# Kernel tuning notes

Hardware: AMD Instinct MI355X
Metric: run time of the kernel (lower is better)

Reference implementation:

```python
import jax, jax.numpy as jnp
import numpy as np

N = 50000   # nodes
E = 640000  # edges
D = 128     # feature dim (din == dmid, required since edge_attr is reused every layer)
L = 5       # GINEConv layers
BN_EPS = 1e-5


def setup_inputs() -> dict:
    key = jax.random.key(0)
    ks = jax.random.split(key, 8)
    x = jax.random.normal(ks[0], (N, D), dtype=jnp.float32)
    edge_index = jax.random.randint(ks[1], (2, E), 0, N, dtype=jnp.int64)
    edge_attr = jax.random.normal(ks[2], (E, D), dtype=jnp.float32)
    W1 = jax.random.normal(ks[3], (L, D, D), dtype=jnp.float32) * 0.05
    b1 = jnp.zeros((L, D), dtype=jnp.float32)
    gamma = jnp.ones((L, D), dtype=jnp.float32)
    beta = jnp.zeros((L, D), dtype=jnp.float32)
    W2 = jax.random.normal(ks[4], (L, D, D), dtype=jnp.float32) * 0.05
    b2 = jnp.zeros((L, D), dtype=jnp.float32)
    return {"x": x, "edge_index": edge_index, "edge_attr": edge_attr,
            "W1": W1, "b1": b1, "gamma": gamma, "beta": beta, "W2": W2, "b2": b2}


def reference(x, edge_index, edge_attr, W1, b1, gamma, beta, W2, b2):
    src, dst = edge_index[0], edge_index[1]  # PyG: messages flow src(j) -> dst(i)
    h = x
    for l in range(L):
        # GINEConv message + aggregate: sum_j ReLU(x_j + e_ij)
        m = jax.nn.relu(h[src] + edge_attr)               # [E, D] gather + add
        agg = jax.ops.segment_sum(m, dst, num_segments=N)  # [N, D] scatter-sum
        h = agg + h  # (1 + eps) * x_i with eps = 0
        # MLP: Linear -> BatchNorm1d (batch stats) -> ReLU -> Linear
        h = h @ W1[l] + b1[l]
        mu = jnp.mean(h, axis=0)
        var = jnp.var(h, axis=0)  # biased var, as torch BN uses for normalization
        h = gamma[l] * (h - mu) * jax.lax.rsqrt(var + BN_EPS) + beta[l]
        h = jax.nn.relu(h)
        h = h @ W2[l] + b2[l]
    return h
```

## Files before the change

kernel.cpp:

```cpp
#include <hip/hip_runtime.h>
#include <hip/hip_bf16.h>
#include <stdint.h>

#define D 128
#define LAYERS 5
#define BN_EPS 1e-5f

typedef unsigned int uint32;
typedef __bf16 bf16x8 __attribute__((ext_vector_type(8)));
typedef float f32x4 __attribute__((ext_vector_type(4)));
typedef float f32x2 __attribute__((ext_vector_type(2)));

__device__ inline unsigned short f2bf(float f) {
    uint32 u = __float_as_uint(f);
    return (unsigned short)((u + 0x7fffu + ((u >> 16) & 1u)) >> 16);
}
__device__ inline float bflo(uint32 p) { return __uint_as_float(p << 16); }
__device__ inline float bfhi(uint32 p) { return __uint_as_float(p & 0xffff0000u); }
__device__ inline uint32 pack2(float a, float b) {
    return (uint32)f2bf(a) | ((uint32)f2bf(b) << 16);
}


__global__ void detect_kernel(const int* __restrict__ ei, int* __restrict__ flag) {
    if (threadIdx.x == 0 && blockIdx.x == 0) {
        int allz = 1;
#pragma unroll
        for (int i = 0; i < 16; ++i) allz &= (ei[2 * i + 1] == 0);
        *flag = allz;
    }
}


__global__ __launch_bounds__(256) void hist_kernel(const int* __restrict__ ei,
                                                   const int* __restrict__ flag,
                                                   int* __restrict__ deg, int E, int n) {
    int e = blockIdx.x * blockDim.x + threadIdx.x;
    if (e >= E) return;
    int is64 = *flag;
    int d = is64 ? ei[2 * ((size_t)E + e)] : ei[E + e];
    if ((unsigned)d < (unsigned)n) atomicAdd(&deg[d], 1);
}

__global__ __launch_bounds__(1024) void scan_kernel(const int* __restrict__ deg,
                                                    int* __restrict__ off, int n) {
    __shared__ int tsum[1024];
    int t = threadIdx.x;
    int CH = (n + 1023) >> 10;
    int lo = t * CH;
    int hi = lo + CH; if (hi > n) hi = n;
    int s = 0;
    for (int i = lo; i < hi; ++i) s += deg[i];
    tsum[t] = s;
    __syncthreads();
    for (int d = 1; d < 1024; d <<= 1) {
        int v = (t >= d) ? tsum[t - d] : 0;
        __syncthreads();
        tsum[t] += v;
        __syncthreads();
    }
    int run = tsum[t] - s;
    for (int i = lo; i < hi; ++i) { off[i] = run; run += deg[i]; }
    if (t == 1023) off[n] = tsum[1023];
}

__global__ __launch_bounds__(256) void fill_kernel(const int* __restrict__ ei,
                                                   const int* __restrict__ flag,
                                                   const int* __restrict__ off,
                                                   int* __restrict__ cursor,
                                                   int* __restrict__ srcs,
                                                   int* __restrict__ eidx, int E, int n) {
    int e = blockIdx.x * blockDim.x + threadIdx.x;
    if (e >= E) return;
    int is64 = *flag;
    int d = is64 ? ei[2 * ((size_t)E + e)] : ei[E + e];
    int s = is64 ? ei[2 * (size_t)e] : ei[e];
    if ((unsigned)d >= (unsigned)n || (unsigned)s >= (unsigned)n) return;
    int p = atomicAdd(&cursor[d], 1);
    int pos = off[d] + p;
    srcs[pos] = s;
    eidx[pos] = e;
}


__global__ __launch_bounds__(256) void agg_cvt_kernel(const float* __restrict__ x,
                                                      const float* __restrict__ ea,
                                                      const int* __restrict__ off,
                                                      const int* __restrict__ srcs,
                                                      const int* __restrict__ eidx,
                                                      uint32* __restrict__ eab,
                                                      uint32* __restrict__ out,
                                                      float* __restrict__ colstats, int n) {
    if (blockIdx.x == 0 && threadIdx.x < 256) colstats[threadIdx.x] = 0.f;
    int node = blockIdx.x * 4 + (threadIdx.x >> 6);
    if (node >= n) return;
    int lane = threadIdx.x & 63;
    int c = lane * 2;
    float2 acc = *(const float2*)(x + (size_t)node * D + c);
    int e = off[node], end = off[node + 1];
    for (; e + 4 <= end; e += 4) {
        int s0 = srcs[e], s1 = srcs[e + 1], s2 = srcs[e + 2], s3 = srcs[e + 3];
        int y0 = eidx[e], y1 = eidx[e + 1], y2 = eidx[e + 2], y3 = eidx[e + 3];
        f32x2 v0 = __builtin_nontemporal_load((const f32x2*)(ea + (size_t)y0 * D + c));
        f32x2 v1 = __builtin_nontemporal_load((const f32x2*)(ea + (size_t)y1 * D + c));
        f32x2 v2 = __builtin_nontemporal_load((const f32x2*)(ea + (size_t)y2 * D + c));
        f32x2 v3 = __builtin_nontemporal_load((const f32x2*)(ea + (size_t)y3 * D + c));
        float2 h0 = *(const float2*)(x + (size_t)s0 * D + c);
        float2 h1 = *(const float2*)(x + (size_t)s1 * D + c);
        float2 h2 = *(const float2*)(x + (size_t)s2 * D + c);
        float2 h3 = *(const float2*)(x + (size_t)s3 * D + c);
        acc.x += fmaxf(h0.x + v0.x, 0.f) + fmaxf(h1.x + v1.x, 0.f)
               + fmaxf(h2.x + v2.x, 0.f) + fmaxf(h3.x + v3.x, 0.f);
        acc.y += fmaxf(h0.y + v0.y, 0.f) + fmaxf(h1.y + v1.y, 0.f)
               + fmaxf(h2.y + v2.y, 0.f) + fmaxf(h3.y + v3.y, 0.f);
        __builtin_nontemporal_store(pack2(v0.x, v0.y), eab + (size_t)e * 64 + lane);
        __builtin_nontemporal_store(pack2(v1.x, v1.y), eab + (size_t)(e + 1) * 64 + lane);
        __builtin_nontemporal_store(pack2(v2.x, v2.y), eab + (size_t)(e + 2) * 64 + lane);
        __builtin_nontemporal_store(pack2(v3.x, v3.y), eab + (size_t)(e + 3) * 64 + lane);
    }
    for (; e < end; ++e) {
        int s0 = srcs[e], y0 = eidx[e];
        float2 v0 = *(const float2*)(ea + (size_t)y0 * D + c);
        float2 h0 = *(const float2*)(x + (size_t)s0 * D + c);
        acc.x += fmaxf(h0.x + v0.x, 0.f);
        acc.y += fmaxf(h0.y + v0.y, 0.f);
        eab[(size_t)e * 64 + lane] = pack2(v0.x, v0.y);
    }
    out[(size_t)node * 64 + lane] = pack2(acc.x, acc.y);
}


__global__ __launch_bounds__(256) void agg_kernel(const uint32* __restrict__ h,
                                                  const uint32* __restrict__ eab,
                                                  const int* __restrict__ off,
                                                  const int* __restrict__ srcs,
                                                  uint32* __restrict__ out,
                                                  float* __restrict__ colstats, int n) {
    if (blockIdx.x == 0 && threadIdx.x < 256) colstats[threadIdx.x] = 0.f;
    int node = blockIdx.x * 4 + (threadIdx.x >> 6);
    if (node >= n) return;
    int lane = threadIdx.x & 63;
    uint32 hn = h[(size_t)node * 64 + lane];
    float2 acc = make_float2(bflo(hn), bfhi(hn));
    int e = off[node], end = off[node + 1];
    for (; e + 4 <= end; e += 4) {
        int s0 = srcs[e], s1 = srcs[e + 1], s2 = srcs[e + 2], s3 = srcs[e + 3];
        uint32 a0 = __builtin_nontemporal_load(eab + (size_t)e * 64 + lane);
        uint32 a1 = __builtin_nontemporal_load(eab + (size_t)(e + 1) * 64 + lane);
        uint32 a2 = __builtin_nontemporal_load(eab + (size_t)(e + 2) * 64 + lane);
        uint32 a3 = __builtin_nontemporal_load(eab + (size_t)(e + 3) * 64 + lane);
        uint32 h0 = h[(size_t)s0 * 64 + lane];
        uint32 h1 = h[(size_t)s1 * 64 + lane];
        uint32 h2 = h[(size_t)s2 * 64 + lane];
        uint32 h3 = h[(size_t)s3 * 64 + lane];
        acc.x += fmaxf(bflo(h0) + bflo(a0), 0.f) + fmaxf(bflo(h1) + bflo(a1), 0.f)
               + fmaxf(bflo(h2) + bflo(a2), 0.f) + fmaxf(bflo(h3) + bflo(a3), 0.f);
        acc.y += fmaxf(bfhi(h0) + bfhi(a0), 0.f) + fmaxf(bfhi(h1) + bfhi(a1), 0.f)
               + fmaxf(bfhi(h2) + bfhi(a2), 0.f) + fmaxf(bfhi(h3) + bfhi(a3), 0.f);
    }
    for (; e < end; ++e) {
        int s0 = srcs[e];
        uint32 a0 = eab[(size_t)e * 64 + lane];
        uint32 h0 = h[(size_t)s0 * 64 + lane];
        acc.x += fmaxf(bflo(h0) + bflo(a0), 0.f);
        acc.y += fmaxf(bfhi(h0) + bfhi(a0), 0.f);
    }
    out[(size_t)node * 64 + lane] = pack2(acc.x, acc.y);
}


__global__ __launch_bounds__(256) void wt_kernel(const float* __restrict__ W1,
                                                 const float* __restrict__ W2,
                                                 unsigned short* __restrict__ wt) {
    int id = blockIdx.x * 256 + threadIdx.x;
    if (id >= 10 * 16384) return;
    int l = id >> 14;
    int rem = id & 16383;
    int nn = rem >> 7, kk = rem & 127;
    const float* base = (l < 5) ? (W1 + (size_t)l * 16384) : (W2 + (size_t)(l - 5) * 16384);
    wt[(size_t)l * 16384 + nn * 128 + kk] = f2bf(base[kk * 128 + nn]);
}


template <int MODE, bool F32OUT>
__global__ __launch_bounds__(256) void gemm_kernel(const uint4* __restrict__ A,
                                                   const uint4* __restrict__ Wt4,
                                                   const float* __restrict__ bias,
                                                   void* __restrict__ outp,
                                                   float* __restrict__ colstats,
                                                   const float* __restrict__ gamma,
                                                   const float* __restrict__ beta,
                                                   float inv_n, int n) {
    __shared__ float red[256];
    const int t = threadIdx.x;
    const int wv = t >> 6, l = t & 63;
    const int lrow = l & 15, lk = l >> 4;
    const int r0 = blockIdx.x * 64 + wv * 16;

    if (MODE == 1) {
        red[t] = 0.f;
    } else {
        if (t < 128) {
            float mu = colstats[t] * inv_n;
            float var = colstats[128 + t] * inv_n - mu * mu;
            float inv = rsqrtf(var + BN_EPS);
            float sc = gamma[t] * inv;
            red[t] = sc;
            red[128 + t] = beta[t] - mu * sc;
        }
    }
    __syncthreads();

    bf16x8 af[4];
    const int arow = r0 + lrow;
    const bool rowok = arow < n;
#pragma unroll
    for (int c = 0; c < 4; ++c) {
        union { uint4 u; bf16x8 v; uint32 w[4]; } bu;
        bu.u = make_uint4(0u, 0u, 0u, 0u);
        if (rowok) bu.u = A[(size_t)arow * 16 + c * 4 + lk];
        if (MODE == 2) {
            const int kb = c * 32 + lk * 8;
            float xv[8];
#pragma unroll
            for (int i = 0; i < 4; ++i) {
                xv[2 * i]     = bflo(bu.w[i]);
                xv[2 * i + 1] = bfhi(bu.w[i]);
            }
#pragma unroll
            for (int j = 0; j < 8; ++j)
                xv[j] = fmaxf(fmaf(red[kb + j], xv[j], red[128 + kb + j]), 0.f);
#pragma unroll
            for (int i = 0; i < 4; ++i)
                bu.w[i] = pack2(xv[2 * i], xv[2 * i + 1]);
        }
        af[c] = bu.v;
    }

    float* outF = (float*)outp;
    unsigned short* outB = (unsigned short*)outp;
    float s[8], s2[8];

#pragma unroll
    for (int n0 = 0; n0 < 8; ++n0) {
        const int wcol = n0 * 16 + lrow;
        f32x4 acc = {0.f, 0.f, 0.f, 0.f};
#pragma unroll
        for (int c = 0; c < 4; ++c) {
            union { uint4 u; bf16x8 v; } bu;
            bu.u = Wt4[wcol * 16 + c * 4 + lk];
            acc = __builtin_amdgcn_mfma_f32_16x16x32_bf16(af[c], bu.v, acc, 0, 0, 0);
        }
        const float bcol = bias[wcol];
        float ls = 0.f, ls2 = 0.f;
#pragma unroll
        for (int r = 0; r < 4; ++r) {
            int row = r0 + lk * 4 + r;
            float v = acc[r] + bcol;
            if (row < n) {
                if (F32OUT) outF[(size_t)row * D + wcol] = v;
                else        outB[(size_t)row * D + wcol] = f2bf(v);
                if (MODE == 1) { ls += v; ls2 += v * v; }
            }
        }
        s[n0] = ls; s2[n0] = ls2;
    }

    if (MODE == 1) {
#pragma unroll
        for (int n0 = 0; n0 < 8; ++n0) {
            const int wcol = n0 * 16 + lrow;
            float ls = s[n0], ls2 = s2[n0];
            ls  += __shfl_xor(ls, 16);  ls  += __shfl_xor(ls, 32);
            ls2 += __shfl_xor(ls2, 16); ls2 += __shfl_xor(ls2, 32);
            if (lk == 0) {
                atomicAdd(&red[wcol], ls);
                atomicAdd(&red[D + wcol], ls2);
            }
        }
        __syncthreads();
        if (t < 128) {
            atomicAdd(&colstats[t], red[t]);
            atomicAdd(&colstats[D + t], red[D + t]);
        }
    }
}


extern "C" void kernel_launch(void* const* d_in, const int* in_sizes, int n_in,
                              void* d_out, int out_size, void* d_ws, size_t ws_size,
                              hipStream_t stream) {
    const float* x      = (const float*)d_in[0];
    const int*   ei     = (const int*)d_in[1];
    const float* ea     = (const float*)d_in[2];
    const float* W1     = (const float*)d_in[3];
    const float* b1     = (const float*)d_in[4];
    const float* gamma  = (const float*)d_in[5];
    const float* beta   = (const float*)d_in[6];
    const float* W2     = (const float*)d_in[7];
    const float* b2     = (const float*)d_in[8];
    const int N = in_sizes[0] / D;
    const int E = in_sizes[1] / 2;

    char* w = (char*)d_ws;
    auto alloc = [&](size_t bytes) {
        char* p = w;
        w += (bytes + 255) & ~(size_t)255;
        return p;
    };
    int*    off      = (int*)alloc((size_t)(N + 1) * sizeof(int));
    int*    deg      = (int*)alloc((size_t)N * sizeof(int));
    int*    cursor   = (int*)alloc((size_t)N * sizeof(int));
    int*    flag     = (int*)alloc(256);
    float*  colstats = (float*)alloc(256 * sizeof(float));
    unsigned short* wt = (unsigned short*)alloc(10 * 16384 * sizeof(unsigned short));
    int*    srcs     = (int*)alloc((size_t)E * sizeof(int));
    int*    eidx     = (int*)alloc((size_t)E * sizeof(int));
    uint32* eab      = (uint32*)alloc((size_t)E * 64 * sizeof(uint32));
    uint32* G        = (uint32*)alloc((size_t)N * 64 * sizeof(uint32));
    uint32* T        = (uint32*)alloc((size_t)N * 64 * sizeof(uint32));
    uint32* H        = (uint32*)alloc((size_t)N * 64 * sizeof(uint32));

    wt_kernel<<<(10 * 16384 + 255) / 256, 256, 0, stream>>>(W1, W2, wt);
    detect_kernel<<<1, 64, 0, stream>>>(ei, flag);
    hipMemsetAsync(deg, 0, (size_t)N * sizeof(int), stream);
    hist_kernel<<<(E + 255) / 256, 256, 0, stream>>>(ei, flag, deg, E, N);
    scan_kernel<<<1, 1024, 0, stream>>>(deg, off, N);
    hipMemsetAsync(cursor, 0, (size_t)N * sizeof(int), stream);
    fill_kernel<<<(E + 255) / 256, 256, 0, stream>>>(ei, flag, off, cursor, srcs, eidx, E, N);

    int gemmBlocks = (N + 63) / 64;
    int aggBlocks  = (N + 3) / 4;
    float inv_n = 1.0f / (float)N;

    for (int l = 0; l < LAYERS; ++l) {
        if (l == 0)
            agg_cvt_kernel<<<aggBlocks, 256, 0, stream>>>(x, ea, off, srcs, eidx, eab, G,
                                                          colstats, N);
        else
            agg_kernel<<<aggBlocks, 256, 0, stream>>>(H, eab, off, srcs, G, colstats, N);
        gemm_kernel<1, false><<<gemmBlocks, 256, 0, stream>>>(
            (const uint4*)G, (const uint4*)(wt + (size_t)l * 16384), b1 + l * D,
            T, colstats, nullptr, nullptr, inv_n, N);
        if (l < LAYERS - 1)
            gemm_kernel<2, false><<<gemmBlocks, 256, 0, stream>>>(
                (const uint4*)T, (const uint4*)(wt + (size_t)(5 + l) * 16384), b2 + l * D,
                H, colstats, gamma + l * D, beta + l * D, inv_n, N);
        else
            gemm_kernel<2, true><<<gemmBlocks, 256, 0, stream>>>(
                (const uint4*)T, (const uint4*)(wt + (size_t)(5 + l) * 16384), b2 + l * D,
                d_out, colstats, gamma + l * D, beta + l * D, inv_n, N);
    }
}
```

Before: 773.6 us.

## Split layer-0 edge conversion into separate streaming kernel and bf16 input

Replaces the fused layer-0 aggregate-and-convert kernel with a dedicated conversion kernel that writes edge attributes to bf16 in CSR order, plus a kernel that converts x to bf16. All layers then use the same bf16 aggregation kernel. Column statistics move to per-layer buffers zeroed by one memset together with the degree and cursor arrays, which removes the in-kernel zeroing and one memset. This adds an extra pass over the edge attributes and x, and layer 0 now aggregates bf16-rounded x.

```diff
diff --git a/kernel.cpp b/kernel.cpp
--- a/kernel.cpp
+++ b/kernel.cpp
@@ -83,50 +83,44 @@
 }
 
 
-__global__ __launch_bounds__(256) void agg_cvt_kernel(const float* __restrict__ x,
-                                                      const float* __restrict__ ea,
-                                                      const int* __restrict__ off,
-                                                      const int* __restrict__ srcs,
-                                                      const int* __restrict__ eidx,
-                                                      uint32* __restrict__ eab,
-                                                      uint32* __restrict__ out,
-                                                      float* __restrict__ colstats, int n) {
-    if (blockIdx.x == 0 && threadIdx.x < 256) colstats[threadIdx.x] = 0.f;
-    int node = blockIdx.x * 4 + (threadIdx.x >> 6);
-    if (node >= n) return;
+__global__ __launch_bounds__(256) void wt_kernel(const float* __restrict__ W1,
+                                                 const float* __restrict__ W2,
+                                                 unsigned short* __restrict__ wt) {
+    int id = blockIdx.x * 256 + threadIdx.x;
+    if (id >= 10 * 16384) return;
+    int l = id >> 14;
+    int rem = id & 16383;
+    int nn = rem >> 7, kk = rem & 127;
+    const float* base = (l < 5) ? (W1 + (size_t)l * 16384) : (W2 + (size_t)(l - 5) * 16384);
+    wt[(size_t)l * 16384 + nn * 128 + kk] = f2bf(base[kk * 128 + nn]);
+}
+
+
+__global__ __launch_bounds__(256) void xb_kernel(const float* __restrict__ x,
+                                                 uint32* __restrict__ xb, int total) {
+    int i = blockIdx.x * 256 + threadIdx.x;
+    if (i >= total) return;
+    f32x2 v = *(const f32x2*)(x + 2 * (size_t)i);
+    xb[i] = pack2(v.x, v.y);
+}
+
+
+__global__ __launch_bounds__(256) void cvt_kernel(const float* __restrict__ ea,
+                                                  const int* __restrict__ eidx,
+                                                  uint32* __restrict__ eab, int E) {
+    int wid = ((blockIdx.x * 256 + threadIdx.x) >> 6) * 2;
     int lane = threadIdx.x & 63;
-    int c = lane * 2;
-    float2 acc = *(const float2*)(x + (size_t)node * D + c);
-    int e = off[node], end = off[node + 1];
-    for (; e + 4 <= end; e += 4) {
-        int s0 = srcs[e], s1 = srcs[e + 1], s2 = srcs[e + 2], s3 = srcs[e + 3];
-        int y0 = eidx[e], y1 = eidx[e + 1], y2 = eidx[e + 2], y3 = eidx[e + 3];
-        f32x2 v0 = __builtin_nontemporal_load((const f32x2*)(ea + (size_t)y0 * D + c));
-        f32x2 v1 = __builtin_nontemporal_load((const f32x2*)(ea + (size_t)y1 * D + c));
-        f32x2 v2 = __builtin_nontemporal_load((const f32x2*)(ea + (size_t)y2 * D + c));
-        f32x2 v3 = __builtin_nontemporal_load((const f32x2*)(ea + (size_t)y3 * D + c));
-        float2 h0 = *(const float2*)(x + (size_t)s0 * D + c);
-        float2 h1 = *(const float2*)(x + (size_t)s1 * D + c);
-        float2 h2 = *(const float2*)(x + (size_t)s2 * D + c);
-        float2 h3 = *(const float2*)(x + (size_t)s3 * D + c);
-        acc.x += fmaxf(h0.x + v0.x, 0.f) + fmaxf(h1.x + v1.x, 0.f)
-               + fmaxf(h2.x + v2.x, 0.f) + fmaxf(h3.x + v3.x, 0.f);
-        acc.y += fmaxf(h0.y + v0.y, 0.f) + fmaxf(h1.y + v1.y, 0.f)
-               + fmaxf(h2.y + v2.y, 0.f) + fmaxf(h3.y + v3.y, 0.f);
-        __builtin_nontemporal_store(pack2(v0.x, v0.y), eab + (size_t)e * 64 + lane);
-        __builtin_nontemporal_store(pack2(v1.x, v1.y), eab + (size_t)(e + 1) * 64 + lane);
-        __builtin_nontemporal_store(pack2(v2.x, v2.y), eab + (size_t)(e + 2) * 64 + lane);
-        __builtin_nontemporal_store(pack2(v3.x, v3.y), eab + (size_t)(e + 3) * 64 + lane);
-    }
-    for (; e < end; ++e) {
-        int s0 = srcs[e], y0 = eidx[e];
-        float2 v0 = *(const float2*)(ea + (size_t)y0 * D + c);
-        float2 h0 = *(const float2*)(x + (size_t)s0 * D + c);
-        acc.x += fmaxf(h0.x + v0.x, 0.f);
-        acc.y += fmaxf(h0.y + v0.y, 0.f);
-        eab[(size_t)e * 64 + lane] = pack2(v0.x, v0.y);
-    }
-    out[(size_t)node * 64 + lane] = pack2(acc.x, acc.y);
+    if (wid >= E) return;
+    int y0 = eidx[wid];
+    f32x2 v0 = __builtin_nontemporal_load((const f32x2*)(ea + (size_t)y0 * D + lane * 2));
+    if (wid + 1 < E) {
+        int y1 = eidx[wid + 1];
+        f32x2 v1 = __builtin_nontemporal_load((const f32x2*)(ea + (size_t)y1 * D + lane * 2));
+        __builtin_nontemporal_store(pack2(v0.x, v0.y), eab + (size_t)wid * 64 + lane);
+        __builtin_nontemporal_store(pack2(v1.x, v1.y), eab + (size_t)(wid + 1) * 64 + lane);
+    } else {
+        __builtin_nontemporal_store(pack2(v0.x, v0.y), eab + (size_t)wid * 64 + lane);
+    }
 }
 
 
@@ -134,9 +128,7 @@
                                                   const uint32* __restrict__ eab,
                                                   const int* __restrict__ off,
                                                   const int* __restrict__ srcs,
-                                                  uint32* __restrict__ out,
-                                                  float* __restrict__ colstats, int n) {
-    if (blockIdx.x == 0 && threadIdx.x < 256) colstats[threadIdx.x] = 0.f;
+                                                  uint32* __restrict__ out, int n) {
     int node = blockIdx.x * 4 + (threadIdx.x >> 6);
     if (node >= n) return;
     int lane = threadIdx.x & 63;
@@ -169,19 +161,6 @@
 }
 
 
-__global__ __launch_bounds__(256) void wt_kernel(const float* __restrict__ W1,
-                                                 const float* __restrict__ W2,
-                                                 unsigned short* __restrict__ wt) {
-    int id = blockIdx.x * 256 + threadIdx.x;
-    if (id >= 10 * 16384) return;
-    int l = id >> 14;
-    int rem = id & 16383;
-    int nn = rem >> 7, kk = rem & 127;
-    const float* base = (l < 5) ? (W1 + (size_t)l * 16384) : (W2 + (size_t)(l - 5) * 16384);
-    wt[(size_t)l * 16384 + nn * 128 + kk] = f2bf(base[kk * 128 + nn]);
-}
-
-
 template <int MODE, bool F32OUT>
 __global__ __launch_bounds__(256) void gemm_kernel(const uint4* __restrict__ A,
                                                    const uint4* __restrict__ Wt4,
@@ -309,46 +288,49 @@
         return p;
     };
     int*    off      = (int*)alloc((size_t)(N + 1) * sizeof(int));
-    int*    deg      = (int*)alloc((size_t)N * sizeof(int));
-    int*    cursor   = (int*)alloc((size_t)N * sizeof(int));
+    int*    zbase    = (int*)alloc(((size_t)2 * N + 5 * 256) * sizeof(int));
+    int*    deg      = zbase;
+    int*    cursor   = zbase + N;
+    float*  colstats = (float*)(zbase + 2 * N);
     int*    flag     = (int*)alloc(256);
-    float*  colstats = (float*)alloc(256 * sizeof(float));
     unsigned short* wt = (unsigned short*)alloc(10 * 16384 * sizeof(unsigned short));
     int*    srcs     = (int*)alloc((size_t)E * sizeof(int));
     int*    eidx     = (int*)alloc((size_t)E * sizeof(int));
     uint32* eab      = (uint32*)alloc((size_t)E * 64 * sizeof(uint32));
+    uint32* xb       = (uint32*)alloc((size_t)N * 64 * sizeof(uint32));
     uint32* G        = (uint32*)alloc((size_t)N * 64 * sizeof(uint32));
     uint32* T        = (uint32*)alloc((size_t)N * 64 * sizeof(uint32));
     uint32* H        = (uint32*)alloc((size_t)N * 64 * sizeof(uint32));
 
     wt_kernel<<<(10 * 16384 + 255) / 256, 256, 0, stream>>>(W1, W2, wt);
     detect_kernel<<<1, 64, 0, stream>>>(ei, flag);
-    hipMemsetAsync(deg, 0, (size_t)N * sizeof(int), stream);
+    hipMemsetAsync(zbase, 0, ((size_t)2 * N + 5 * 256) * sizeof(int), stream);
     hist_kernel<<<(E + 255) / 256, 256, 0, stream>>>(ei, flag, deg, E, N);
     scan_kernel<<<1, 1024, 0, stream>>>(deg, off, N);
-    hipMemsetAsync(cursor, 0, (size_t)N * sizeof(int), stream);
     fill_kernel<<<(E + 255) / 256, 256, 0, stream>>>(ei, flag, off, cursor, srcs, eidx, E, N);
-
-    int gemmBlocks = (N + 63) / 64;
-    int aggBlocks  = (N + 3) / 4;
-    float inv_n = 1.0f / (float)N;
-
+    xb_kernel<<<(N * 64 + 255) / 256, 256, 0, stream>>>(x, xb, N * 64);
+    cvt_kernel<<<(E + 7) / 8, 256, 0, stream>>>(ea, eidx, eab, E);
+
+    const int gemmBlocks = (N + 63) / 64;
+    const int aggBlocks  = (N + 3) / 4;
+    const float inv_n = 1.0f / (float)N;
+
+    const uint32* hin = xb;
     for (int l = 0; l < LAYERS; ++l) {
-        if (l == 0)
-            agg_cvt_kernel<<<aggBlocks, 256, 0, stream>>>(x, ea, off, srcs, eidx, eab, G,
-                                                          colstats, N);
-        else
-            agg_kernel<<<aggBlocks, 256, 0, stream>>>(H, eab, off, srcs, G, colstats, N);
+        float* cst = colstats + l * 256;
+        const uint4* wt1 = (const uint4*)(wt + (size_t)l * 16384);
+        const uint4* wt2 = (const uint4*)(wt + (size_t)(5 + l) * 16384);
+        agg_kernel<<<aggBlocks, 256, 0, stream>>>(hin, eab, off, srcs, G, N);
         gemm_kernel<1, false><<<gemmBlocks, 256, 0, stream>>>(
-            (const uint4*)G, (const uint4*)(wt + (size_t)l * 16384), b1 + l * D,
-            T, colstats, nullptr, nullptr, inv_n, N);
+            (const uint4*)G, wt1, b1 + l * D, T, cst, nullptr, nullptr, inv_n, N);
         if (l < LAYERS - 1)
             gemm_kernel<2, false><<<gemmBlocks, 256, 0, stream>>>(
-                (const uint4*)T, (const uint4*)(wt + (size_t)(5 + l) * 16384), b2 + l * D,
-                H, colstats, gamma + l * D, beta + l * D, inv_n, N);
+                (const uint4*)T, wt2, b2 + l * D, H, cst,
+                gamma + l * D, beta + l * D, inv_n, N);
         else
             gemm_kernel<2, true><<<gemmBlocks, 256, 0, stream>>>(
-                (const uint4*)T, (const uint4*)(wt + (size_t)(5 + l) * 16384), b2 + l * D,
-                d_out, colstats, gamma + l * D, beta + l * D, inv_n, N);
-    }
-}
+                (const uint4*)T, wt2, b2 + l * D, d_out, cst,
+                gamma + l * D, beta + l * D, inv_n, N);
+        hin = H;
+    }
+}
```

After: 849.3 us. +9.8%, slower.
